# Kernel optimization log

Measured on AMD Instinct MI355X. Metric: run time of the kernel, lower is better.

Reference implementation:

```python
import jax, jax.numpy as jnp
import numpy as np

KB, KI = 6, 0   # kernel quantizer: quantized_bits(6, 0, alpha=1)
BB, BI = 6, 0   # bias quantizer:   quantized_bits(6, 0, alpha=1)
AB, AI = 6, 0   # activation:       quantized_relu(6, 0)


def _round_ste(p):
    # straight-through round (QKeras _round_through); tf.round and jnp.round
    # both round half-to-even
    return p + jax.lax.stop_gradient(jnp.round(p) - p)


def quantized_bits(x, bits, integer):
    # QKeras quantized_bits with keep_negative=1, symmetric=0, alpha=1
    m = float(2 ** (bits - 1))      # non-sign levels
    m_i = float(2 ** integer)
    p = x * (m / m_i)
    return (m_i / m) * jnp.clip(_round_ste(p), -m, m - 1.0)


def quantized_relu(x, bits, integer):
    # QKeras quantized_relu with negative_slope=0, use_sigmoid=0
    m = float(2 ** bits)
    m_i = float(2 ** integer)
    p = x * (m / m_i)
    return (m_i / m) * jnp.clip(_round_ste(p), 0.0, m - 1.0)


def setup_inputs() -> dict:
    key = jax.random.key(0)
    ks = jax.random.split(key, 9)
    dims = [128, 1024, 2048, 4096, 4096]
    inp = {"x": jax.random.normal(ks[0], (8192, dims[0]), dtype=jnp.float32)}
    for i in range(4):
        fan_in, fan_out = dims[i], dims[i + 1]
        scale = np.sqrt(2.0 / (fan_in + fan_out))  # glorot-ish scale
        inp[f"W{i}"] = jax.random.normal(ks[1 + 2 * i], (fan_in, fan_out), dtype=jnp.float32) * scale
        inp[f"b{i}"] = jax.random.normal(ks[2 + 2 * i], (fan_out,), dtype=jnp.float32) * 0.01
    return inp


def reference(x, W0, b0, W1, b1, W2, b2, W3, b3):
    Ws = [W0, W1, W2, W3]
    bs = [b0, b1, b2, b3]
    h = x
    for i in range(4):
        wq = quantized_bits(Ws[i], KB, KI)
        bq = quantized_bits(bs[i], BB, BI)
        h = jnp.dot(h, wq) + bq
        if i != 3:  # last layer has activation=None
            h = quantized_relu(h, AB, AI)
    return h
```

## Files before the change

kernel.cpp:

```cpp
#include <hip/hip_runtime.h>
#include <stdint.h>

typedef int v4i __attribute__((ext_vector_type(4)));

__device__ __forceinline__ float qlevel(float x) {
  float p = rintf(x * 32.0f);
  return fminf(fmaxf(p, -32.0f), 31.0f);
}

__device__ __forceinline__ int8_t qrelu_level(float p) {
  int q = (int)rintf(p);
  q = q < 0 ? 0 : (q > 63 ? 63 : q);
  return (int8_t)q;
}

__device__ __forceinline__ void async16(const void* g, void* l) {
  __builtin_amdgcn_global_load_lds(
      (const __attribute__((address_space(1))) void*)g,
      (__attribute__((address_space(3))) void*)l, 16, 0, 0);
}

__global__ __launch_bounds__(256) void quant_w0_k(const float* __restrict__ W,
                                                  int8_t* __restrict__ wq) {
  int i = blockIdx.x * 256 + threadIdx.x;
  float4 v = ((const float4*)W)[i];
  char4 c;
  c.x = (int8_t)(int)qlevel(v.x);
  c.y = (int8_t)(int)qlevel(v.y);
  c.z = (int8_t)(int)qlevel(v.z);
  c.w = (int8_t)(int)qlevel(v.w);
  ((char4*)wq)[i] = c;
}

__global__ __launch_bounds__(256) void quantT_k(const float* __restrict__ W,
                                                int8_t* __restrict__ wt,
                                                int K, int N) {
  const int t = threadIdx.x;
  const int l = t & 63;
  const int kc = t >> 6;
  const int k0 = blockIdx.y * 64 + kc * 16;
  const int n = blockIdx.x * 64 + l;
  union { int8_t b[16]; int4 v; } u;
#pragma unroll
  for (int j = 0; j < 16; ++j)
    u.b[j] = (int8_t)(int)qlevel(W[(size_t)(k0 + j) * N + n]);
  *(int4*)&wt[(size_t)n * K + k0] = u.v;
}

__global__ __launch_bounds__(256) void quant_bias_k(
    const float* __restrict__ b0, const float* __restrict__ b1,
    const float* __restrict__ b2, const float* __restrict__ b3,
    float* __restrict__ o0, float* __restrict__ o1,
    float* __restrict__ o2, float* __restrict__ o3) {
  int i = blockIdx.x * 256 + threadIdx.x;
  if (i < 1024) o0[i] = qlevel(b0[i]);
  if (i < 2048) o1[i] = qlevel(b1[i]);
  o2[i] = qlevel(b2[i]);
  o3[i] = qlevel(b3[i]);
}

__global__ __launch_bounds__(256) void layer0_k(const float* __restrict__ x,
                                                const int8_t* __restrict__ w0q,
                                                const float* __restrict__ bint,
                                                int8_t* __restrict__ a1) {
  const int K = 128, N = 1024;
  __shared__ float xs[64][132];
  __shared__ int8_t wsm[128][64];
  const int tid = threadIdx.x;
  const int m0 = blockIdx.y * 64;
  const int n0 = blockIdx.x * 64;
#pragma unroll
  for (int i = 0; i < 8; ++i) {
    int idx = tid + 256 * i;
    int row = idx >> 5, c4 = idx & 31;
    float4 v = *(const float4*)(x + (size_t)(m0 + row) * K + c4 * 4);
    *(float4*)&xs[row][c4 * 4] = v;
  }
#pragma unroll
  for (int i = 0; i < 8; ++i) {
    int idx = tid + 256 * i;
    int k = idx >> 4, c4 = idx & 15;
    *(int*)&wsm[k][c4 * 4] = *(const int*)(w0q + (size_t)k * N + n0 + c4 * 4);
  }
  __syncthreads();
  const int ty = tid >> 4, tx = tid & 15;
  float acc[4][4] = {};
  for (int k4 = 0; k4 < K; k4 += 4) {
    float xr[4][4];
#pragma unroll
    for (int i = 0; i < 4; ++i) {
      float4 v = *(const float4*)&xs[ty * 4 + i][k4];
      xr[i][0] = v.x; xr[i][1] = v.y; xr[i][2] = v.z; xr[i][3] = v.w;
    }
#pragma unroll
    for (int kk = 0; kk < 4; ++kk) {
      char4 cv = *(const char4*)&wsm[k4 + kk][tx * 4];
      float w0 = (float)cv.x, w1 = (float)cv.y, w2 = (float)cv.z, w3 = (float)cv.w;
#pragma unroll
      for (int i = 0; i < 4; ++i) {
        acc[i][0] = fmaf(xr[i][kk], w0, acc[i][0]);
        acc[i][1] = fmaf(xr[i][kk], w1, acc[i][1]);
        acc[i][2] = fmaf(xr[i][kk], w2, acc[i][2]);
        acc[i][3] = fmaf(xr[i][kk], w3, acc[i][3]);
      }
    }
  }
  const int n = n0 + tx * 4;
  float b0v = 2.0f * bint[n + 0], b1v = 2.0f * bint[n + 1];
  float b2v = 2.0f * bint[n + 2], b3v = 2.0f * bint[n + 3];
#pragma unroll
  for (int i = 0; i < 4; ++i) {
    int m = m0 + ty * 4 + i;
    char4 o;
    o.x = qrelu_level(2.0f * acc[i][0] + b0v);
    o.y = qrelu_level(2.0f * acc[i][1] + b1v);
    o.z = qrelu_level(2.0f * acc[i][2] + b2v);
    o.w = qrelu_level(2.0f * acc[i][3] + b3v);
    *(char4*)&a1[(size_t)m * 1024 + n] = o;
  }
}

template <bool FINAL>
__global__ __launch_bounds__(256) void gemm_i8(const int8_t* __restrict__ A,
                                               const int8_t* __restrict__ BT,
                                               const float* __restrict__ bint,
                                               void* __restrict__ outp,
                                               int M, int N, int K) {
  __shared__ __align__(16) int8_t ldsA[2][64 * 128];
  __shared__ __align__(16) int8_t ldsB[2][64 * 128];
  const int tid = threadIdx.x;
  const int wid = tid >> 6;
  const int lane = tid & 63;
  const int wm = wid >> 1, wn = wid & 1;
  const int quad = lane >> 4, r = lane & 15;
  const int m0 = blockIdx.y * 128, n0 = blockIdx.x * 128;

  const int8_t* Ab = A + (size_t)m0 * K;
  const int8_t* Bb = BT + (size_t)n0 * K;

  const int srow = tid >> 2;
  const int sp = tid & 3;
  const int skc = (sp - (srow >> 1)) & 3;
  const int8_t* gA0 = Ab + (size_t)srow * K + skc * 16;
  const int8_t* gA1 = Ab + (size_t)(srow + 64) * K + skc * 16;
  const int8_t* gB0 = Bb + (size_t)srow * K + skc * 16;
  const int8_t* gB1 = Bb + (size_t)(srow + 64) * K + skc * 16;
  const int ldsOff0 = (wid * 64) * 16;
  const int ldsOff1 = (wid * 64 + 256) * 16;

  const int pfrag = (quad + (r >> 1)) & 3;

  v4i acc[4][4] = {};

  async16(gA0, &ldsA[0][ldsOff0]);
  async16(gA1, &ldsA[0][ldsOff1]);
  async16(gB0, &ldsB[0][ldsOff0]);
  async16(gB1, &ldsB[0][ldsOff1]);
  __syncthreads();

  for (int k0 = 0; k0 < K; k0 += 64) {
    const int p = (k0 >> 6) & 1;
    if (k0 + 64 < K) {
      async16(gA0 + k0 + 64, &ldsA[1 - p][ldsOff0]);
      async16(gA1 + k0 + 64, &ldsA[1 - p][ldsOff1]);
      async16(gB0 + k0 + 64, &ldsB[1 - p][ldsOff0]);
      async16(gB1 + k0 + 64, &ldsB[1 - p][ldsOff1]);
    }
    v4i af[4], bf[4];
#pragma unroll
    for (int mt = 0; mt < 4; ++mt)
      af[mt] = *(const v4i*)&ldsA[p][(wm * 64 + mt * 16 + r) * 64 + pfrag * 16];
#pragma unroll
    for (int nt = 0; nt < 4; ++nt)
      bf[nt] = *(const v4i*)&ldsB[p][(wn * 64 + nt * 16 + r) * 64 + pfrag * 16];
#pragma unroll
    for (int mt = 0; mt < 4; ++mt)
#pragma unroll
      for (int nt = 0; nt < 4; ++nt)
        acc[mt][nt] = __builtin_amdgcn_mfma_i32_16x16x64_i8(af[mt], bf[nt],
                                                            acc[mt][nt], 0, 0, 0);
    __syncthreads();
  }

  const int mbase = m0 + wm * 64;
  const int nbase = n0 + wn * 64;
  if (FINAL) {
    float* out = (float*)outp;
#pragma unroll
    for (int nt = 0; nt < 4; ++nt) {
      int n = nbase + nt * 16 + r;
      float bq = bint[n] * 0.03125f;
#pragma unroll
      for (int mt = 0; mt < 4; ++mt)
#pragma unroll
        for (int g = 0; g < 4; ++g) {
          int m = mbase + mt * 16 + quad * 4 + g;
          out[(size_t)m * N + n] = (float)acc[mt][nt][g] * (1.0f / 2048.0f) + bq;
        }
    }
  } else {
    int8_t* out = (int8_t*)outp;
#pragma unroll
    for (int nt = 0; nt < 4; ++nt) {
      int n = nbase + nt * 16 + r;
      float b2 = 2.0f * bint[n];
#pragma unroll
      for (int mt = 0; mt < 4; ++mt)
#pragma unroll
        for (int g = 0; g < 4; ++g) {
          int m = mbase + mt * 16 + quad * 4 + g;
          out[(size_t)m * N + n] =
              qrelu_level((float)acc[mt][nt][g] * 0.03125f + b2);
        }
    }
  }
}

extern "C" void kernel_launch(void* const* d_in, const int* in_sizes, int n_in,
                              void* d_out, int out_size, void* d_ws, size_t ws_size,
                              hipStream_t stream) {
  const float* x  = (const float*)d_in[0];
  const float* W0 = (const float*)d_in[1];
  const float* b0 = (const float*)d_in[2];
  const float* W1 = (const float*)d_in[3];
  const float* b1 = (const float*)d_in[4];
  const float* W2 = (const float*)d_in[5];
  const float* b2 = (const float*)d_in[6];
  const float* W3 = (const float*)d_in[7];
  const float* b3 = (const float*)d_in[8];

  uint8_t* ws = (uint8_t*)d_ws;
  int8_t* wq0 = (int8_t*)(ws + 0);
  int8_t* wt1 = (int8_t*)(ws + 131072);
  int8_t* wt2 = (int8_t*)(ws + 2228224);
  int8_t* wt3 = (int8_t*)(ws + 10616832);
  float*  bq0 = (float*)(ws + 27394048);
  float*  bq1 = (float*)(ws + 27398144);
  float*  bq2 = (float*)(ws + 27406336);
  float*  bq3 = (float*)(ws + 27422720);
  int8_t* a1  = (int8_t*)(ws + 27439104);
  int8_t* a2  = (int8_t*)(ws + 35827712);
  int8_t* a3  = (int8_t*)(ws + 52604928);

  quant_w0_k<<<128, 256, 0, stream>>>(W0, wq0);
  quantT_k<<<dim3(2048 / 64, 1024 / 64), 256, 0, stream>>>(W1, wt1, 1024, 2048);
  quantT_k<<<dim3(4096 / 64, 2048 / 64), 256, 0, stream>>>(W2, wt2, 2048, 4096);
  quantT_k<<<dim3(4096 / 64, 4096 / 64), 256, 0, stream>>>(W3, wt3, 4096, 4096);
  quant_bias_k<<<16, 256, 0, stream>>>(b0, b1, b2, b3, bq0, bq1, bq2, bq3);
  layer0_k<<<dim3(16, 128), 256, 0, stream>>>(x, wq0, bq0, a1);
  gemm_i8<false><<<dim3(16, 64), 256, 0, stream>>>(a1, wt1, bq1, a2, 8192, 2048, 1024);
  gemm_i8<false><<<dim3(32, 64), 256, 0, stream>>>(a2, wt2, bq2, a3, 8192, 4096, 2048);
  gemm_i8<true><<<dim3(32, 64), 256, 0, stream>>>(a3, wt3, bq3, d_out, 8192, 4096, 4096);
}
```

Before: 521.2 us.

## Triple-buffer LDS tiles in int8 GEMM with vmcnt waits and one barrier

Turns the double-buffered async global-to-LDS pipeline into a three-stage ring buffer that prefetches two K-tiles ahead. Each iteration waits with an explicit s_waitcnt vmcnt(4) and a single s_barrier, replacing the end-of-loop __syncthreads. This gives the loads more time to hide latency and removes one barrier per iteration, at the cost of 50% more LDS per block, which can lower occupancy. Correctness relies on the hand-counted vmcnt values and on a barrier before each buffer is reused.

```diff
diff --git a/kernel.cpp b/kernel.cpp
--- a/kernel.cpp
+++ b/kernel.cpp
@@ -126,8 +126,8 @@
                                                const float* __restrict__ bint,
                                                void* __restrict__ outp,
                                                int M, int N, int K) {
-  __shared__ __align__(16) int8_t ldsA[2][64 * 128];
-  __shared__ __align__(16) int8_t ldsB[2][64 * 128];
+  __shared__ __align__(16) int8_t ldsA[3][128 * 64];
+  __shared__ __align__(16) int8_t ldsB[3][128 * 64];
   const int tid = threadIdx.x;
   const int wid = tid >> 6;
   const int lane = tid & 63;
@@ -141,45 +141,56 @@
   const int srow = tid >> 2;
   const int sp = tid & 3;
   const int skc = (sp - (srow >> 1)) & 3;
-  const int8_t* gA0 = Ab + (size_t)srow * K + skc * 16;
-  const int8_t* gA1 = Ab + (size_t)(srow + 64) * K + skc * 16;
-  const int8_t* gB0 = Bb + (size_t)srow * K + skc * 16;
-  const int8_t* gB1 = Bb + (size_t)(srow + 64) * K + skc * 16;
+  const int8_t* gA = Ab + (size_t)srow * K + skc * 16;
+  const int8_t* gB = Bb + (size_t)srow * K + skc * 16;
+  const size_t rstep = (size_t)64 * K;
   const int ldsOff0 = (wid * 64) * 16;
   const int ldsOff1 = (wid * 64 + 256) * 16;
+  int8_t* ldsAf = &ldsA[0][0];
+  int8_t* ldsBf = &ldsB[0][0];
 
   const int pfrag = (quad + (r >> 1)) & 3;
 
   v4i acc[4][4] = {};
 
-  async16(gA0, &ldsA[0][ldsOff0]);
-  async16(gA1, &ldsA[0][ldsOff1]);
-  async16(gB0, &ldsB[0][ldsOff0]);
-  async16(gB1, &ldsB[0][ldsOff1]);
-  __syncthreads();
-
+  async16(gA,         ldsAf + ldsOff0);
+  async16(gA + rstep, ldsAf + ldsOff1);
+  async16(gB,         ldsBf + ldsOff0);
+  async16(gB + rstep, ldsBf + ldsOff1);
+  async16(gA + 64,         ldsAf + 8192 + ldsOff0);
+  async16(gA + 64 + rstep, ldsAf + 8192 + ldsOff1);
+  async16(gB + 64,         ldsBf + 8192 + ldsOff0);
+  async16(gB + 64 + rstep, ldsBf + 8192 + ldsOff1);
+
+  int pr = 0;
   for (int k0 = 0; k0 < K; k0 += 64) {
-    const int p = (k0 >> 6) & 1;
-    if (k0 + 64 < K) {
-      async16(gA0 + k0 + 64, &ldsA[1 - p][ldsOff0]);
-      async16(gA1 + k0 + 64, &ldsA[1 - p][ldsOff1]);
-      async16(gB0 + k0 + 64, &ldsB[1 - p][ldsOff0]);
-      async16(gB1 + k0 + 64, &ldsB[1 - p][ldsOff1]);
+    if (k0 + 64 < K) asm volatile("s_waitcnt vmcnt(4)" ::: "memory");
+    else             asm volatile("s_waitcnt vmcnt(0)" ::: "memory");
+    asm volatile("s_barrier" ::: "memory");
+    if (k0 + 128 < K) {
+      int pw = pr + 2; if (pw >= 3) pw -= 3;
+      const int kb = k0 + 128;
+      async16(gA + kb,         ldsAf + pw * 8192 + ldsOff0);
+      async16(gA + kb + rstep, ldsAf + pw * 8192 + ldsOff1);
+      async16(gB + kb,         ldsBf + pw * 8192 + ldsOff0);
+      async16(gB + kb + rstep, ldsBf + pw * 8192 + ldsOff1);
     }
     v4i af[4], bf[4];
 #pragma unroll
     for (int mt = 0; mt < 4; ++mt)
-      af[mt] = *(const v4i*)&ldsA[p][(wm * 64 + mt * 16 + r) * 64 + pfrag * 16];
+      af[mt] = *(const v4i*)(ldsAf + pr * 8192 +
+                             (wm * 64 + mt * 16 + r) * 64 + pfrag * 16);
 #pragma unroll
     for (int nt = 0; nt < 4; ++nt)
-      bf[nt] = *(const v4i*)&ldsB[p][(wn * 64 + nt * 16 + r) * 64 + pfrag * 16];
+      bf[nt] = *(const v4i*)(ldsBf + pr * 8192 +
+                             (wn * 64 + nt * 16 + r) * 64 + pfrag * 16);
 #pragma unroll
     for (int mt = 0; mt < 4; ++mt)
 #pragma unroll
       for (int nt = 0; nt < 4; ++nt)
         acc[mt][nt] = __builtin_amdgcn_mfma_i32_16x16x64_i8(af[mt], bf[nt],
                                                             acc[mt][nt], 0, 0, 0);
-    __syncthreads();
+    pr = pr + 1; if (pr == 3) pr = 0;
   }
 
   const int mbase = m0 + wm * 64;
```

After: 521.8 us. Within noise of the previous version (+0.1%).
